# Kernel tuning notes

Hardware: AMD Instinct MI355X
Metric: run time of the kernel (lower is better)

The kernel has to match this reference:

```python
import jax, jax.numpy as jnp
import numpy as np

NUM_EMBED = 1024
NUM_HEADS = 16
BLOCK_SIZE = 2048


def setup_inputs() -> dict:
    key = jax.random.key(0)
    k1, k2, k3, k4, k5 = jax.random.split(key, 5)
    C = NUM_EMBED
    s = 1.0 / np.sqrt(C)
    x = jax.random.normal(k1, (2, BLOCK_SIZE, C), dtype=jnp.float32)
    # nn.Linear params: weight (out,in), bias (out,)
    w_attn = jax.random.uniform(k2, (3 * C, C), minval=-s, maxval=s, dtype=jnp.float32)
    b_attn = jax.random.uniform(k3, (3 * C,), minval=-s, maxval=s, dtype=jnp.float32)
    w_proj = jax.random.uniform(k4, (C, C), minval=-s, maxval=s, dtype=jnp.float32)
    b_proj = jax.random.uniform(k5, (C,), minval=-s, maxval=s, dtype=jnp.float32)
    return {"x": x, "w_attn": w_attn, "b_attn": b_attn, "w_proj": w_proj, "b_proj": b_proj}


def reference(x, w_attn, b_attn, w_proj, b_proj):
    B, T, C = x.shape
    H = NUM_HEADS
    D = C // H
    kqv = jnp.einsum('btc,oc->bto', x, w_attn) + b_attn  # (B,T,3C)
    # Original code splits as K, Q, V in that order.
    K, Q, V = jnp.split(kqv, 3, axis=2)
    K = K.reshape(B, T, H, D).transpose(0, 2, 1, 3)  # (B,H,T,D)
    Q = Q.reshape(B, T, H, D).transpose(0, 2, 1, 3)
    V = V.reshape(B, T, H, D).transpose(0, 2, 1, 3)
    aff = jnp.einsum('bhqd,bhkd->bhqk', Q, K) * (D ** -0.5)  # (B,H,T,T)
    causal = jnp.tril(jnp.ones((T, T), dtype=bool))
    aff = jnp.where(causal[None, None], aff, jnp.float32(-jnp.inf))
    wei = jax.nn.softmax(aff, axis=-1)
    attn = jnp.einsum('bhqk,bhkd->bhqd', wei, V)
    attn = attn.transpose(0, 2, 1, 3).reshape(B, T, C)
    out = jnp.einsum('btc,oc->bto', attn, w_proj) + b_proj
    return out
```

## Files before the change

### kernel.cpp

```cpp
#include <hip/hip_runtime.h>
#include <hip/hip_bf16.h>
#include <cstdint>

typedef __attribute__((ext_vector_type(8))) short bf16x8;
typedef __attribute__((ext_vector_type(4))) float f32x4;
typedef __attribute__((ext_vector_type(4))) uint16_t u16x4;

__device__ __forceinline__ uint16_t f2b(float f) {
  union { float f; uint32_t i; } v; v.f = f;
  return (uint16_t)((v.i + 0x7FFFu + ((v.i >> 16) & 1u)) >> 16);
}

#define GLDS16(g, l) __builtin_amdgcn_global_load_lds( \
    (const __attribute__((address_space(1))) void*)(g), \
    (__attribute__((address_space(3))) void*)(l), 16, 0, 0)

__global__ __launch_bounds__(256) void cvt_all(
    const float* __restrict__ x, const float* __restrict__ wa, const float* __restrict__ wp,
    uint16_t* __restrict__ xb, uint16_t* __restrict__ wab, uint16_t* __restrict__ wpb) {
  const int i = (blockIdx.x * 256 + threadIdx.x) * 4;
  const float* src; uint16_t* dst; int off;
  if (i < 4194304)      { src = x;  dst = xb;  off = i; }
  else if (i < 7340032) { src = wa; dst = wab; off = i - 4194304; }
  else                  { src = wp; dst = wpb; off = i - 7340032; }
  const float4 v = *(const float4*)(src + off);
  u16x4 o;
  o.x = f2b(v.x); o.y = f2b(v.y); o.z = f2b(v.z); o.w = f2b(v.w);
  *(u16x4*)(dst + off) = o;
}

template <int BM, bool OUT_BF16>
__global__ __launch_bounds__(256) void gemm_bt_bias(
    const uint16_t* __restrict__ A, const uint16_t* __restrict__ B,
    const float* __restrict__ bias, void* __restrict__ Cv,
    int M, int N, int K) {
  constexpr int MI = BM / 32;
  constexpr int CA = BM / 16;
  constexpr int CPW = (2 * (CA + 8)) / 4;
  constexpr int CT_PITCH = OUT_BF16 ? 72 : 68;
  constexpr size_t CT_BYTES = (size_t)4 * (BM / 2) * CT_PITCH * (OUT_BF16 ? 2 : 4);
  constexpr size_t ST_BYTES = (size_t)(2 * (BM * 32 + 4096)) * 2;
  constexpr size_t LB = CT_BYTES > ST_BYTES ? CT_BYTES : ST_BYTES;
  __shared__ alignas(16) unsigned char ldsb[LB];
  uint16_t* lds = (uint16_t*)ldsb;
  const int offB0 = BM * 32;
  const int offA1 = BM * 32 + 4096;
  const int offB1 = 2 * BM * 32 + 4096;

  const int tid = threadIdx.x;
  const int wave = tid >> 6, lane = tid & 63;
  const int q4 = lane >> 4, l16 = lane & 15;
  const int wm = wave >> 1, wn = wave & 1;
  const long blockM = (long)blockIdx.y * BM;
  const long blockN = (long)blockIdx.x * 128;

  f32x4 acc[MI][4] = {};

  for (int k0 = 0; k0 < K; k0 += 64) {
#pragma unroll
    for (int c = 0; c < CPW; ++c) {
      const int id = c * 4 + wave;
      const uint16_t* mat; long rowBase; int a, kk, off;
      if (id < CA)               { mat = A; rowBase = blockM; a = id;            kk = k0;      off = 0; }
      else if (id < CA + 8)      { mat = B; rowBase = blockN; a = id - CA;       kk = k0;      off = offB0; }
      else if (id < 2 * CA + 8)  { mat = A; rowBase = blockM; a = id - CA - 8;   kk = k0 + 32; off = offA1; }
      else                       { mat = B; rowBase = blockN; a = id - 2*CA - 8; kk = k0 + 32; off = offB1; }
      const int flat = a * 64 + lane;
      const int row = flat >> 2, seg = flat & 3;
      GLDS16(mat + (rowBase + row) * (long)K + kk + seg * 8, lds + off + a * 512);
    }
    __syncthreads();
#pragma unroll
    for (int h = 0; h < 2; ++h) {
      const uint16_t* Ah = lds + (h ? offA1 : 0);
      const uint16_t* Bh = lds + (h ? offB1 : offB0);
      bf16x8 af[MI], bfr[4];
#pragma unroll
      for (int i = 0; i < MI; ++i)
        af[i] = *(const bf16x8*)&Ah[(wm * (BM / 2) + i * 16 + l16) * 32 + q4 * 8];
#pragma unroll
      for (int j = 0; j < 4; ++j)
        bfr[j] = *(const bf16x8*)&Bh[(wn * 64 + j * 16 + l16) * 32 + q4 * 8];
#pragma unroll
      for (int i = 0; i < MI; ++i)
#pragma unroll
        for (int j = 0; j < 4; ++j)
          acc[i][j] = __builtin_amdgcn_mfma_f32_16x16x32_bf16(af[i], bfr[j], acc[i][j], 0, 0, 0);
    }
    __syncthreads();
  }

  if (OUT_BF16) {
    uint16_t* ct = lds + wave * (BM / 2) * 72;
#pragma unroll
    for (int j = 0; j < 4; ++j) {
      const float bv = bias[blockN + wn * 64 + j * 16 + l16];
#pragma unroll
      for (int i = 0; i < MI; ++i)
#pragma unroll
        for (int r = 0; r < 4; ++r)
          ct[(i * 16 + q4 * 4 + r) * 72 + j * 16 + l16] = f2b(acc[i][j][r] + bv);
    }
    __syncthreads();
    uint16_t* Cb = (uint16_t*)Cv;
#pragma unroll
    for (int st = 0; st < BM / 16; ++st) {
      const int flat = st * 64 + lane;
      const int row = flat >> 3, seg = flat & 7;
      const bf16x8 v = *(const bf16x8*)&ct[row * 72 + seg * 8];
      *(bf16x8*)&Cb[(blockM + wm * (BM / 2) + row) * (long)N + blockN + wn * 64 + seg * 8] = v;
    }
  } else {
    float* ct = (float*)ldsb + wave * (BM / 2) * 68;
#pragma unroll
    for (int j = 0; j < 4; ++j) {
      const float bv = bias[blockN + wn * 64 + j * 16 + l16];
#pragma unroll
      for (int i = 0; i < MI; ++i)
#pragma unroll
        for (int r = 0; r < 4; ++r)
          ct[(i * 16 + q4 * 4 + r) * 68 + j * 16 + l16] = acc[i][j][r] + bv;
    }
    __syncthreads();
    float* Cb = (float*)Cv;
#pragma unroll
    for (int st = 0; st < BM / 8; ++st) {
      const int flat = st * 64 + lane;
      const int row = flat >> 4, seg = flat & 15;
      const f32x4 v = *(const f32x4*)&ct[row * 68 + seg * 4];
      *(f32x4*)&Cb[(blockM + wm * (BM / 2) + row) * (long)N + blockN + wn * 64 + seg * 4] = v;
    }
  }
}

__global__ __launch_bounds__(256, 2) void attn_flash(
    const uint16_t* __restrict__ kqv, uint16_t* __restrict__ attn) {
  constexpr int T = 2048, C = 1024, C3 = 3072;
  __shared__ uint16_t KP[128 * 72];
  __shared__ uint16_t Vt[64 * 136];
  uint32_t* VtW = (uint32_t*)Vt;

  const int tid = threadIdx.x;
  const int wave = tid >> 6, lane = tid & 63;
  const int q4 = lane >> 4, l16 = lane & 15;
  const int p = blockIdx.x >> 5, bh = blockIdx.x & 31;
  const int b = bh >> 4, h = bh & 15;
  const size_t base = (size_t)b * T * C3;
  const int hD = h * 64;

  uint16_t* Pt = &KP[wave * 2176];

  const int tr = tid >> 3, kch = tid & 7;
  const float sc = 0.125f * 1.4426950408889634f;

  for (int ss = 0; ss < 2; ++ss) {
    const int qb = ss ? p : 31 - p;
    const int nkt = (qb >> 1) + 1;
    const int qrow = qb * 64 + wave * 16 + l16;
    const bf16x8 qf0 = *(const bf16x8*)&kqv[base + (size_t)qrow * C3 + C + hD + q4 * 8];
    const bf16x8 qf1 = *(const bf16x8*)&kqv[base + (size_t)qrow * C3 + C + hD + 32 + q4 * 8];

    f32x4 o[4] = {};
    float m_i = -1e30f, l_i = 0.f;

    bf16x8 pk[4], pv0[2], pv1[2];
#pragma unroll
    for (int rr = 0; rr < 4; ++rr)
      pk[rr] = *(const bf16x8*)&kqv[base + (size_t)(rr * 32 + tr) * C3 + hD + kch * 8];
#pragma unroll
    for (int s2 = 0; s2 < 2; ++s2) {
      const size_t g = base + (size_t)(2 * (s2 * 32 + tr)) * C3 + 2 * C + hD + kch * 8;
      pv0[s2] = *(const bf16x8*)&kqv[g];
      pv1[s2] = *(const bf16x8*)&kqv[g + C3];
    }

    for (int kt = 0; kt < nkt; ++kt) {
      const int kbase = kt * 128;
      __syncthreads();
#pragma unroll
      for (int rr = 0; rr < 4; ++rr)
        *(bf16x8*)&KP[(rr * 32 + tr) * 72 + kch * 8] = pk[rr];
#pragma unroll
      for (int s2 = 0; s2 < 2; ++s2) {
        const int colw = ((s2 * 32 + tr) + 8 * kch) & 63;
        const uint32_t* a0 = (const uint32_t*)&pv0[s2];
        const uint32_t* a1 = (const uint32_t*)&pv1[s2];
#pragma unroll
        for (int i = 0; i < 8; ++i) {
          const uint32_t w = (i & 1)
              ? __builtin_amdgcn_perm(a1[i >> 1], a0[i >> 1], 0x07060302u)
              : __builtin_amdgcn_perm(a1[i >> 1], a0[i >> 1], 0x05040100u);
          VtW[(kch * 8 + i) * 68 + colw] = w;
        }
      }
      __syncthreads();
      if (kt + 1 < nkt) {
        const int kb = kbase + 128;
#pragma unroll
        for (int rr = 0; rr < 4; ++rr)
          pk[rr] = *(const bf16x8*)&kqv[base + (size_t)(kb + rr * 32 + tr) * C3 + hD + kch * 8];
#pragma unroll
        for (int s2 = 0; s2 < 2; ++s2) {
          const size_t g = base + (size_t)(kb + 2 * (s2 * 32 + tr)) * C3 + 2 * C + hD + kch * 8;
          pv0[s2] = *(const bf16x8*)&kqv[g];
          pv1[s2] = *(const bf16x8*)&kqv[g + C3];
        }
      }
      f32x4 s[8];
#pragma unroll
      for (int nk = 0; nk < 8; ++nk) {
        f32x4 z = {};
        const bf16x8 kf0 = *(const bf16x8*)&KP[(nk * 16 + l16) * 72 + q4 * 8];
        const bf16x8 kf1 = *(const bf16x8*)&KP[(nk * 16 + l16) * 72 + 32 + q4 * 8];
        z = __builtin_amdgcn_mfma_f32_16x16x32_bf16(kf0, qf0, z, 0, 0, 0);
        z = __builtin_amdgcn_mfma_f32_16x16x32_bf16(kf1, qf1, z, 0, 0, 0);
        s[nk] = z;
      }
      if (kbase + 127 > qb * 64 + wave * 16) {
#pragma unroll
        for (int nk = 0; nk < 8; ++nk) {
          const int key0 = kbase + nk * 16 + q4 * 4;
#pragma unroll
          for (int r = 0; r < 4; ++r)
            s[nk][r] = (key0 + r <= qrow) ? s[nk][r] : -1e30f;
        }
      }
      float mloc = s[0][0];
#pragma unroll
      for (int nk = 0; nk < 8; ++nk)
#pragma unroll
        for (int r = 0; r < 4; ++r) mloc = fmaxf(mloc, s[nk][r]);
      mloc = fmaxf(mloc, __shfl_xor(mloc, 16, 64));
      mloc = fmaxf(mloc, __shfl_xor(mloc, 32, 64));
      const float mnew = fmaxf(m_i, mloc * sc);
      const float alpha = exp2f(m_i - mnew);
      const bool mchg = mnew > m_i;
      m_i = mnew;
      float rs = 0.f;
#pragma unroll
      for (int nk = 0; nk < 8; ++nk)
#pragma unroll
        for (int r = 0; r < 4; ++r) {
          const float pe = exp2f(fmaf(s[nk][r], sc, -mnew));
          s[nk][r] = pe;
          rs += pe;
        }
      rs += __shfl_xor(rs, 16, 64);
      rs += __shfl_xor(rs, 32, 64);
      l_i = l_i * alpha + rs;
      if (__any(mchg)) {
#pragma unroll
        for (int r = 0; r < 4; ++r) {
          const float ar = __shfl(alpha, q4 * 4 + r, 64);
#pragma unroll
          for (int d4 = 0; d4 < 4; ++d4) o[d4][r] *= ar;
        }
      }
      __syncthreads();
#pragma unroll
      for (int nk = 0; nk < 8; ++nk) {
        union { __hip_bfloat162 h2; uint32_t u; } c01, c23;
        c01.h2 = __float22bfloat162_rn(make_float2(s[nk][0], s[nk][1]));
        c23.h2 = __float22bfloat162_rn(make_float2(s[nk][2], s[nk][3]));
        uint2 pkw; pkw.x = c01.u; pkw.y = c23.u;
        *(uint2*)&Pt[l16 * 136 + nk * 16 + q4 * 4] = pkw;
      }
      __syncthreads();
#pragma unroll
      for (int ks = 0; ks < 4; ++ks) {
        const bf16x8 pf = *(const bf16x8*)&Pt[l16 * 136 + ks * 32 + q4 * 8];
#pragma unroll
        for (int d4 = 0; d4 < 4; ++d4) {
          const int d = d4 * 16 + l16;
          const int col = (ks * 32 + q4 * 8 + 16 * (d >> 3)) & 127;
          const bf16x8 vf = *(const bf16x8*)&Vt[d * 136 + col];
          o[d4] = __builtin_amdgcn_mfma_f32_16x16x32_bf16(pf, vf, o[d4], 0, 0, 0);
        }
      }
    }
    const size_t obase = (size_t)b * T * C;
    const float linv = 1.0f / l_i;
#pragma unroll
    for (int r = 0; r < 4; ++r) {
      const float lr = __shfl(linv, q4 * 4 + r, 64);
      const int q = qb * 64 + wave * 16 + q4 * 4 + r;
      const size_t rowoff = obase + (size_t)q * C + hD;
#pragma unroll
      for (int d4 = 0; d4 < 4; ++d4)
        attn[rowoff + d4 * 16 + l16] = f2b(o[d4][r] * lr);
    }
  }
}

extern "C" void kernel_launch(void* const* d_in, const int* in_sizes, int n_in,
                              void* d_out, int out_size, void* d_ws, size_t ws_size,
                              hipStream_t stream) {
  const float* x      = (const float*)d_in[0];
  const float* w_attn = (const float*)d_in[1];
  const float* b_attn = (const float*)d_in[2];
  const float* w_proj = (const float*)d_in[3];
  const float* b_proj = (const float*)d_in[4];
  float* out = (float*)d_out;

  uint16_t* xb    = (uint16_t*)d_ws;
  uint16_t* wab   = xb  + (size_t)4096 * 1024;
  uint16_t* wpb   = wab + (size_t)3072 * 1024;
  uint16_t* kqv   = wpb + (size_t)1024 * 1024;
  uint16_t* attnb = kqv + (size_t)4096 * 3072;

  dim3 blk(256, 1, 1);
  hipLaunchKernelGGL(cvt_all, dim3(8192), blk, 0, stream, x, w_attn, w_proj, xb, wab, wpb);

  hipLaunchKernelGGL((gemm_bt_bias<128, true>), dim3(3072 / 128, 4096 / 128, 1), blk, 0, stream,
                     xb, wab, b_attn, (void*)kqv, 4096, 3072, 1024);
  hipLaunchKernelGGL(attn_flash, dim3(512, 1, 1), blk, 0, stream, kqv, attnb);
  hipLaunchKernelGGL((gemm_bt_bias<64, false>), dim3(1024 / 128, 4096 / 64, 1), blk, 0, stream,
                     attnb, wpb, b_proj, (void*)out, 4096, 1024, 1024);
}
```

Before: 193.6 us.

## Load K fragments directly from global, double-buffer V/P, shrink GEMM K-step

In attention, K tiles now load straight from global memory into MFMA register fragments instead of being staged through LDS. V transpose and P buffers are double-buffered so one barrier per iteration can be dropped, and the register prefetch of the next tile is removed. In the GEMM, the K step per iteration goes from 64 to 32, which halves LDS staging but doubles the number of barriers. The risks are exposed global latency from losing the prefetch, non-coalesced K loads, and more synchronisation in the GEMM.

```diff
diff --git a/kernel.cpp b/kernel.cpp
--- a/kernel.cpp
+++ b/kernel.cpp
@@ -35,17 +35,15 @@
     const float* __restrict__ bias, void* __restrict__ Cv,
     int M, int N, int K) {
   constexpr int MI = BM / 32;
-  constexpr int CA = BM / 16;
-  constexpr int CPW = (2 * (CA + 8)) / 4;
-  constexpr int CT_PITCH = OUT_BF16 ? 72 : 68;
-  constexpr size_t CT_BYTES = (size_t)4 * (BM / 2) * CT_PITCH * (OUT_BF16 ? 2 : 4);
-  constexpr size_t ST_BYTES = (size_t)(2 * (BM * 32 + 4096)) * 2;
+  constexpr int CHA = BM / 16;
+  constexpr int CPW = (CHA + 8) / 4;
+  constexpr size_t ST_BYTES = (size_t)(BM + 128) * 32 * 2;
+  constexpr size_t CT_BYTES = OUT_BF16 ? (size_t)4 * (BM / 2) * 72 * 2
+                                       : (size_t)4 * (BM / 2) * 68 * 4;
   constexpr size_t LB = CT_BYTES > ST_BYTES ? CT_BYTES : ST_BYTES;
   __shared__ alignas(16) unsigned char ldsb[LB];
   uint16_t* lds = (uint16_t*)ldsb;
-  const int offB0 = BM * 32;
-  const int offA1 = BM * 32 + 4096;
-  const int offB1 = 2 * BM * 32 + 4096;
+  const int offB = BM * 32;
 
   const int tid = threadIdx.x;
   const int wave = tid >> 6, lane = tid & 63;
@@ -56,37 +54,32 @@
 
   f32x4 acc[MI][4] = {};
 
-  for (int k0 = 0; k0 < K; k0 += 64) {
+  for (int k0 = 0; k0 < K; k0 += 32) {
 #pragma unroll
     for (int c = 0; c < CPW; ++c) {
       const int id = c * 4 + wave;
-      const uint16_t* mat; long rowBase; int a, kk, off;
-      if (id < CA)               { mat = A; rowBase = blockM; a = id;            kk = k0;      off = 0; }
-      else if (id < CA + 8)      { mat = B; rowBase = blockN; a = id - CA;       kk = k0;      off = offB0; }
-      else if (id < 2 * CA + 8)  { mat = A; rowBase = blockM; a = id - CA - 8;   kk = k0 + 32; off = offA1; }
-      else                       { mat = B; rowBase = blockN; a = id - 2*CA - 8; kk = k0 + 32; off = offB1; }
+      const bool isB = id >= CHA;
+      const int a = isB ? id - CHA : id;
+      const uint16_t* mat = isB ? B : A;
+      const long rowBase = isB ? blockN : blockM;
+      const int off = isB ? offB : 0;
       const int flat = a * 64 + lane;
       const int row = flat >> 2, seg = flat & 3;
-      GLDS16(mat + (rowBase + row) * (long)K + kk + seg * 8, lds + off + a * 512);
-    }
-    __syncthreads();
-#pragma unroll
-    for (int h = 0; h < 2; ++h) {
-      const uint16_t* Ah = lds + (h ? offA1 : 0);
-      const uint16_t* Bh = lds + (h ? offB1 : offB0);
-      bf16x8 af[MI], bfr[4];
-#pragma unroll
-      for (int i = 0; i < MI; ++i)
-        af[i] = *(const bf16x8*)&Ah[(wm * (BM / 2) + i * 16 + l16) * 32 + q4 * 8];
+      GLDS16(mat + (rowBase + row) * (long)K + k0 + seg * 8, lds + off + a * 512);
+    }
+    __syncthreads();
+    bf16x8 af[MI], bfr[4];
+#pragma unroll
+    for (int i = 0; i < MI; ++i)
+      af[i] = *(const bf16x8*)&lds[(wm * (BM / 2) + i * 16 + l16) * 32 + q4 * 8];
+#pragma unroll
+    for (int j = 0; j < 4; ++j)
+      bfr[j] = *(const bf16x8*)&lds[offB + (wn * 64 + j * 16 + l16) * 32 + q4 * 8];
+#pragma unroll
+    for (int i = 0; i < MI; ++i)
 #pragma unroll
       for (int j = 0; j < 4; ++j)
-        bfr[j] = *(const bf16x8*)&Bh[(wn * 64 + j * 16 + l16) * 32 + q4 * 8];
-#pragma unroll
-      for (int i = 0; i < MI; ++i)
-#pragma unroll
-        for (int j = 0; j < 4; ++j)
-          acc[i][j] = __builtin_amdgcn_mfma_f32_16x16x32_bf16(af[i], bfr[j], acc[i][j], 0, 0, 0);
-    }
+        acc[i][j] = __builtin_amdgcn_mfma_f32_16x16x32_bf16(af[i], bfr[j], acc[i][j], 0, 0, 0);
     __syncthreads();
   }
 
@@ -136,9 +129,8 @@
 __global__ __launch_bounds__(256, 2) void attn_flash(
     const uint16_t* __restrict__ kqv, uint16_t* __restrict__ attn) {
   constexpr int T = 2048, C = 1024, C3 = 3072;
-  __shared__ uint16_t KP[128 * 72];
-  __shared__ uint16_t Vt[64 * 136];
-  uint32_t* VtW = (uint32_t*)Vt;
+  __shared__ alignas(16) uint16_t Vt[2][64 * 136];
+  __shared__ alignas(16) uint16_t Pt[2][4 * 2176];
 
   const int tid = threadIdx.x;
   const int wave = tid >> 6, lane = tid & 63;
@@ -147,11 +139,9 @@
   const int b = bh >> 4, h = bh & 15;
   const size_t base = (size_t)b * T * C3;
   const int hD = h * 64;
-
-  uint16_t* Pt = &KP[wave * 2176];
-
-  const int tr = tid >> 3, kch = tid & 7;
   const float sc = 0.125f * 1.4426950408889634f;
+
+  int cb = 0;
 
   for (int ss = 0; ss < 2; ++ss) {
     const int qb = ss ? p : 31 - p;
@@ -163,57 +153,40 @@
     f32x4 o[4] = {};
     float m_i = -1e30f, l_i = 0.f;
 
-    bf16x8 pk[4], pv0[2], pv1[2];
-#pragma unroll
-    for (int rr = 0; rr < 4; ++rr)
-      pk[rr] = *(const bf16x8*)&kqv[base + (size_t)(rr * 32 + tr) * C3 + hD + kch * 8];
-#pragma unroll
-    for (int s2 = 0; s2 < 2; ++s2) {
-      const size_t g = base + (size_t)(2 * (s2 * 32 + tr)) * C3 + 2 * C + hD + kch * 8;
-      pv0[s2] = *(const bf16x8*)&kqv[g];
-      pv1[s2] = *(const bf16x8*)&kqv[g + C3];
-    }
-
     for (int kt = 0; kt < nkt; ++kt) {
       const int kbase = kt * 128;
-      __syncthreads();
-#pragma unroll
-      for (int rr = 0; rr < 4; ++rr)
-        *(bf16x8*)&KP[(rr * 32 + tr) * 72 + kch * 8] = pk[rr];
+      uint32_t* VtW = (uint32_t*)Vt[cb];
 #pragma unroll
       for (int s2 = 0; s2 < 2; ++s2) {
-        const int colw = ((s2 * 32 + tr) + 8 * kch) & 63;
-        const uint32_t* a0 = (const uint32_t*)&pv0[s2];
-        const uint32_t* a1 = (const uint32_t*)&pv1[s2];
+        const int s = s2 * 256 + tid;
+        const int rp = s >> 3, ch = s & 7;
+        const size_t g = base + (size_t)(kbase + 2 * rp) * C3 + 2 * C + hD + ch * 8;
+        const bf16x8 v0 = *(const bf16x8*)&kqv[g];
+        const bf16x8 v1 = *(const bf16x8*)&kqv[g + C3];
+        const int colw = (rp + 8 * ch) & 63;
+        const uint32_t* a0 = (const uint32_t*)&v0;
+        const uint32_t* a1 = (const uint32_t*)&v1;
 #pragma unroll
         for (int i = 0; i < 8; ++i) {
           const uint32_t w = (i & 1)
               ? __builtin_amdgcn_perm(a1[i >> 1], a0[i >> 1], 0x07060302u)
               : __builtin_amdgcn_perm(a1[i >> 1], a0[i >> 1], 0x05040100u);
-          VtW[(kch * 8 + i) * 68 + colw] = w;
-        }
-      }
-      __syncthreads();
-      if (kt + 1 < nkt) {
-        const int kb = kbase + 128;
-#pragma unroll
-        for (int rr = 0; rr < 4; ++rr)
-          pk[rr] = *(const bf16x8*)&kqv[base + (size_t)(kb + rr * 32 + tr) * C3 + hD + kch * 8];
-#pragma unroll
-        for (int s2 = 0; s2 < 2; ++s2) {
-          const size_t g = base + (size_t)(kb + 2 * (s2 * 32 + tr)) * C3 + 2 * C + hD + kch * 8;
-          pv0[s2] = *(const bf16x8*)&kqv[g];
-          pv1[s2] = *(const bf16x8*)&kqv[g + C3];
-        }
+          VtW[(ch * 8 + i) * 68 + colw] = w;
+        }
+      }
+      bf16x8 kf[8][2];
+#pragma unroll
+      for (int nk = 0; nk < 8; ++nk) {
+        const uint16_t* kr = &kqv[base + (size_t)(kbase + nk * 16 + l16) * C3 + hD + q4 * 8];
+        kf[nk][0] = *(const bf16x8*)kr;
+        kf[nk][1] = *(const bf16x8*)(kr + 32);
       }
       f32x4 s[8];
 #pragma unroll
       for (int nk = 0; nk < 8; ++nk) {
         f32x4 z = {};
-        const bf16x8 kf0 = *(const bf16x8*)&KP[(nk * 16 + l16) * 72 + q4 * 8];
-        const bf16x8 kf1 = *(const bf16x8*)&KP[(nk * 16 + l16) * 72 + 32 + q4 * 8];
-        z = __builtin_amdgcn_mfma_f32_16x16x32_bf16(kf0, qf0, z, 0, 0, 0);
-        z = __builtin_amdgcn_mfma_f32_16x16x32_bf16(kf1, qf1, z, 0, 0, 0);
+        z = __builtin_amdgcn_mfma_f32_16x16x32_bf16(kf[nk][0], qf0, z, 0, 0, 0);
+        z = __builtin_amdgcn_mfma_f32_16x16x32_bf16(kf[nk][1], qf1, z, 0, 0, 0);
         s[nk] = z;
       }
       if (kbase + 127 > qb * 64 + wave * 16) {
@@ -256,27 +229,28 @@
           for (int d4 = 0; d4 < 4; ++d4) o[d4][r] *= ar;
         }
       }
-      __syncthreads();
+      uint16_t* Pw = &Pt[cb][wave * 2176];
 #pragma unroll
       for (int nk = 0; nk < 8; ++nk) {
         union { __hip_bfloat162 h2; uint32_t u; } c01, c23;
         c01.h2 = __float22bfloat162_rn(make_float2(s[nk][0], s[nk][1]));
         c23.h2 = __float22bfloat162_rn(make_float2(s[nk][2], s[nk][3]));
         uint2 pkw; pkw.x = c01.u; pkw.y = c23.u;
-        *(uint2*)&Pt[l16 * 136 + nk * 16 + q4 * 4] = pkw;
+        *(uint2*)&Pw[l16 * 136 + nk * 16 + q4 * 4] = pkw;
       }
       __syncthreads();
 #pragma unroll
       for (int ks = 0; ks < 4; ++ks) {
-        const bf16x8 pf = *(const bf16x8*)&Pt[l16 * 136 + ks * 32 + q4 * 8];
+        const bf16x8 pf = *(const bf16x8*)&Pw[l16 * 136 + ks * 32 + q4 * 8];
 #pragma unroll
         for (int d4 = 0; d4 < 4; ++d4) {
           const int d = d4 * 16 + l16;
           const int col = (ks * 32 + q4 * 8 + 16 * (d >> 3)) & 127;
-          const bf16x8 vf = *(const bf16x8*)&Vt[d * 136 + col];
+          const bf16x8 vf = *(const bf16x8*)&Vt[cb][d * 136 + col];
           o[d4] = __builtin_amdgcn_mfma_f32_16x16x32_bf16(pf, vf, o[d4], 0, 0, 0);
         }
       }
+      cb ^= 1;
     }
     const size_t obase = (size_t)b * T * C;
     const float linv = 1.0f / l_i;
```

Result: slower. 215.7 us (+11.5%).
